# Optimization experiments

Hardware: AMD Instinct MI355X
Metric: run time of the kernel (lower is better)

Reference implementation:

```python
import jax, jax.numpy as jnp
import numpy as np
from jax import lax

B, L, H = 32, 512, 1024
PRED_LEN = 32
LN_EPS = 1e-5


def setup_inputs() -> dict:
    key = jax.random.key(0)
    k1, k2, k3 = jax.random.split(key, 3)
    x = jax.random.normal(k1, (B, L, H), dtype=jnp.float32)
    # scale recurrent/input weights by 1/sqrt(H) so the linear recurrence stays finite
    Wxh = jax.random.normal(k2, (H, H), dtype=jnp.float32) / jnp.sqrt(jnp.float32(H))
    Whh = jax.random.normal(k3, (H, H), dtype=jnp.float32) / jnp.sqrt(jnp.float32(H))
    ln_w = jnp.ones((H,), dtype=jnp.float32)
    ln_b = jnp.zeros((H,), dtype=jnp.float32)
    return {"x": x, "Wxh": Wxh, "Whh": Whh, "ln_w": ln_w, "ln_b": ln_b, "pred_len": PRED_LEN}


def _layer_norm(y, w, b):
    mu = jnp.mean(y, axis=-1, keepdims=True)
    var = jnp.mean(jnp.square(y - mu), axis=-1, keepdims=True)
    return (y - mu) * lax.rsqrt(var + LN_EPS) * w + b


def reference(x, Wxh, Whh, ln_w, ln_b, pred_len):
    b, l, h = x.shape
    # precompute input projections for all timesteps: x_t @ Wxh^T (nn.Linear convention)
    xW = jnp.einsum('blh,kh->lbk', x, Wxh)  # [L, B, H]
    WhhT = Whh.T

    def rec_step(h_t, xw_t):
        h_t = xw_t + h_t @ WhhT
        return h_t, h_t

    h0 = jnp.zeros((b, h), dtype=x.dtype)
    h_last, rec = lax.scan(rec_step, h0, xW)
    rec = jnp.transpose(rec, (1, 0, 2))  # [B, L, H]

    def pred_step(h_t, _):
        h_t = h_t @ WhhT
        return h_t, h_t

    _, outs = lax.scan(pred_step, h_last, None, length=pred_len)
    outs = jnp.transpose(outs, (1, 0, 2))  # [B, pred_len, H]
    outputs = _layer_norm(outs, ln_w, ln_b)
    return rec, outputs
```

## Files before the change

kernel.cpp:

```cpp
#include <hip/hip_runtime.h>

#define BB 32
#define LL 512
#define HH 1024
#define PRED 32
#define CC 16
#define NC (LL / CC)
#define C8 8
#define NC8 (LL / C8)
#define LN_EPS 1e-5f

typedef short bf16x8 __attribute__((ext_vector_type(8)));
typedef short s16x4  __attribute__((ext_vector_type(4)));
typedef float f32x4  __attribute__((ext_vector_type(4)));

static __device__ __forceinline__ void split3(float x, short& h, short& m, short& l) {
    unsigned u = __float_as_uint(x);
    unsigned rh = (u + 0x7fffu + ((u >> 16) & 1u)) & 0xffff0000u;
    h = (short)(rh >> 16);
    float x1 = x - __uint_as_float(rh);
    unsigned u1 = __float_as_uint(x1);
    unsigned rm = (u1 + 0x7fffu + ((u1 >> 16) & 1u)) & 0xffff0000u;
    m = (short)(rm >> 16);
    float x2 = x1 - __uint_as_float(rm);
    unsigned u2 = __float_as_uint(x2);
    unsigned rl = (u2 + 0x7fffu + ((u2 >> 16) & 1u)) & 0xffff0000u;
    l = (short)(rl >> 16);
}

static __device__ __forceinline__ void split2(float x, short& h, short& m) {
    unsigned u = __float_as_uint(x);
    unsigned rh = (u + 0x7fffu + ((u >> 16) & 1u)) & 0xffff0000u;
    h = (short)(rh >> 16);
    float x1 = x - __uint_as_float(rh);
    unsigned u1 = __float_as_uint(x1);
    unsigned rm = (u1 + 0x7fffu + ((u1 >> 16) & 1u)) & 0xffff0000u;
    m = (short)(rm >> 16);
}

#define MFMA6(ACC, AH, AM, AL, BH, BM, BL) \
    ACC = __builtin_amdgcn_mfma_f32_16x16x32_bf16(AL, BH, ACC, 0, 0, 0); \
    ACC = __builtin_amdgcn_mfma_f32_16x16x32_bf16(AH, BL, ACC, 0, 0, 0); \
    ACC = __builtin_amdgcn_mfma_f32_16x16x32_bf16(AM, BM, ACC, 0, 0, 0); \
    ACC = __builtin_amdgcn_mfma_f32_16x16x32_bf16(AM, BH, ACC, 0, 0, 0); \
    ACC = __builtin_amdgcn_mfma_f32_16x16x32_bf16(AH, BM, ACC, 0, 0, 0); \
    ACC = __builtin_amdgcn_mfma_f32_16x16x32_bf16(AH, BH, ACC, 0, 0, 0);

__global__ __launch_bounds__(256) void transpose_k(const float* __restrict__ in,
                                                   float* __restrict__ out) {
    __shared__ float tile[32][33];
    int bx = blockIdx.x * 32, by = blockIdx.y * 32;
    int tx = threadIdx.x, ty = threadIdx.y;
    #pragma unroll
    for (int i = 0; i < 32; i += 8)
        tile[ty + i][tx] = in[(size_t)(by + ty + i) * HH + bx + tx];
    __syncthreads();
    #pragma unroll
    for (int i = 0; i < 32; i += 8)
        out[(size_t)(bx + ty + i) * HH + by + tx] = tile[tx][ty + i];
}
// ... 103 lines not shown
            vh0[j] = h; vm0[j] = m;
            split2(xs[j + 8], h, m);
            vh1[j] = h; vm1[j] = m;
        }
        *(bf16x8*)&As2[0][ar][akc]     = vh0;
        *(bf16x8*)&As2[0][ar][akc + 8] = vh1;
        *(bf16x8*)&As2[1][ar][akc]     = vm0;
        *(bf16x8*)&As2[1][ar][akc + 8] = vm1;
        *(bf16x8*)&Bs2[bp][bnr][bkh]     = rb0;
        *(bf16x8*)&Bs2[bp][bnr][bkh + 8] = rb1;
        __syncthreads();
        if (kt + 32 < HH) {
            const float* An = Arow + kt + 32;
            av0 = *(const float4*)(An);
            av1 = *(const float4*)(An + 4);
            av2 = *(const float4*)(An + 8);
            av3 = *(const float4*)(An + 12);
            const short* Bn = Brow + kt + 32;
            rb0 = *(const bf16x8*)(Bn);
            rb1 = *(const bf16x8*)(Bn + 8);
        }
        bf16x8 ah[2], am[2];
        #pragma unroll
        for (int i = 0; i < 2; ++i) {
            ah[i] = *(const bf16x8*)&As2[0][w * 32 + i * 16 + fr][fk];
            am[i] = *(const bf16x8*)&As2[1][w * 32 + i * 16 + fr][fk];
        }
        #pragma unroll
        for (int j = 0; j < 4; ++j) {
            bf16x8 bh = *(const bf16x8*)&Bs2[0][j * 16 + fr][fk];
            bf16x8 bm = *(const bf16x8*)&Bs2[1][j * 16 + fr][fk];
            #pragma unroll
            for (int i = 0; i < 2; ++i) {
                f32x4 a = acc[i][j];
                a = __builtin_amdgcn_mfma_f32_16x16x32_bf16(am[i], bm, a, 0, 0, 0);
                a = __builtin_amdgcn_mfma_f32_16x16x32_bf16(am[i], bh, a, 0, 0, 0);
                a = __builtin_amdgcn_mfma_f32_16x16x32_bf16(ah[i], bm, a, 0, 0, 0);
                a = __builtin_amdgcn_mfma_f32_16x16x32_bf16(ah[i], bh, a, 0, 0, 0);
                acc[i][j] = a;
            }
        }
        __syncthreads();
    }
    const int orow = (lane >> 4) * 4;
    #pragma unroll
    for (int i = 0; i < 2; ++i)
        #pragma unroll
        for (int j = 0; j < 4; ++j) {
            int c = n0 + j * 16 + fr;
            #pragma unroll
            for (int reg = 0; reg < 4; ++reg) {
                int r = m0 + w * 32 + i * 16 + orow + reg;
                C[(size_t)r * HH + c] = acc[i][j][reg];
            }
        }
}

__global__ __launch_bounds__(128) void step_p(
    const short* __restrict__ SA, long sab, long sac, long psA,
    const short* __restrict__ SB,
    float* __restrict__ O, long sob, long soc, int add,
    float* __restrict__ P, long spb, long spc,
    short* __restrict__ S, long ssb, long ssc, long psS) {
    const size_t HM = (size_t)HH * HH;
    __shared__ __align__(16) short As[3][32][40];
    __shared__ __align__(16) short Bs[3][64][40];
    const int tid = threadIdx.x;
    const int lane = tid & 63;
    const int w = tid >> 6;
    const int n0 = blockIdx.x * 64;
    const int m0 = blockIdx.y * 32;
    const int ar = tid >> 2;
    const int akc = (tid & 3) * 8;
    const int agr = m0 + ar;
    const short* Arow = SA + (long)(agr & 31) * sab + (long)(agr >> 5) * sac + akc;
    const int bnr = tid & 63;
    const int bkh = (tid >> 6) * 16;
    const short* Brow = SB + (size_t)(n0 + bnr) * HH + bkh;
    const int fr = lane & 15;
    const int fk = (lane >> 4) * 8;

    f32x4 acc00 = 0, acc01 = 0, acc10 = 0, acc11 = 0;

    bf16x8 ra0 = *(const bf16x8*)(Arow);
    bf16x8 ra1 = *(const bf16x8*)(Arow + psA);
    bf16x8 ra2 = *(const bf16x8*)(Arow + 2 * psA);
    bf16x8 rb0 = *(const bf16x8*)(Brow);
    bf16x8 rb1 = *(const bf16x8*)(Brow + 8);
    bf16x8 rb2 = *(const bf16x8*)(Brow + HM);
    bf16x8 rb3 = *(const bf16x8*)(Brow + HM + 8);
    bf16x8 rb4 = *(const bf16x8*)(Brow + 2 * HM);
    bf16x8 rb5 = *(const bf16x8*)(Brow + 2 * HM + 8);

    for (int kt = 0; kt < HH; kt += 32) {
        *(bf16x8*)&As[0][ar][akc] = ra0;
        *(bf16x8*)&As[1][ar][akc] = ra1;
        *(bf16x8*)&As[2][ar][akc] = ra2;
        *(bf16x8*)&Bs[0][bnr][bkh] = rb0;
        *(bf16x8*)&Bs[0][bnr][bkh + 8] = rb1;
        *(bf16x8*)&Bs[1][bnr][bkh] = rb2;
        *(bf16x8*)&Bs[1][bnr][bkh + 8] = rb3;
        *(bf16x8*)&Bs[2][bnr][bkh] = rb4;
        *(bf16x8*)&Bs[2][bnr][bkh + 8] = rb5;
        __syncthreads();
        if (kt + 32 < HH) {
            const short* An = Arow + kt + 32;
            const short* Bn = Brow + kt + 32;
            ra0 = *(const bf16x8*)(An);
            ra1 = *(const bf16x8*)(An + psA);
            ra2 = *(const bf16x8*)(An + 2 * psA);
            rb0 = *(const bf16x8*)(Bn);
            rb1 = *(const bf16x8*)(Bn + 8);
            rb2 = *(const bf16x8*)(Bn + HM);
            rb3 = *(const bf16x8*)(Bn + HM + 8);
            rb4 = *(const bf16x8*)(Bn + 2 * HM);
            rb5 = *(const bf16x8*)(Bn + 2 * HM + 8);
        }
        bf16x8 a00 = *(const bf16x8*)&As[0][fr][fk];
        bf16x8 a01 = *(const bf16x8*)&As[0][16 + fr][fk];
        bf16x8 a10 = *(const bf16x8*)&As[1][fr][fk];
        bf16x8 a11 = *(const bf16x8*)&As[1][16 + fr][fk];
        bf16x8 a20 = *(const bf16x8*)&As[2][fr][fk];
        bf16x8 a21 = *(const bf16x8*)&As[2][16 + fr][fk];
        bf16x8 b00 = *(const bf16x8*)&Bs[0][w * 32 + fr][fk];
        bf16x8 b01 = *(const bf16x8*)&Bs[0][w * 32 + 16 + fr][fk];
        bf16x8 b10 = *(const bf16x8*)&Bs[1][w * 32 + fr][fk];
        bf16x8 b11 = *(const bf16x8*)&Bs[1][w * 32 + 16 + fr][fk];
        bf16x8 b20 = *(const bf16x8*)&Bs[2][w * 32 + fr][fk];
        bf16x8 b21 = *(const bf16x8*)&Bs[2][w * 32 + 16 + fr][fk];
        MFMA6(acc00, a00, a10, a20, b00, b10, b20)
        MFMA6(acc01, a00, a10, a20, b01, b11, b21)
        MFMA6(acc10, a01, a11, a21, b00, b10, b20)
        MFMA6(acc11, a01, a11, a21, b01, b11, b21)
        __syncthreads();
    }
    const int orow = (lane >> 4) * 4;
    #pragma unroll
    for (int mf = 0; mf < 2; ++mf) {
        #pragma unroll
        for (int nf = 0; nf < 2; ++nf) {
            f32x4 v = mf == 0 ? (nf == 0 ? acc00 : acc01) : (nf == 0 ? acc10 : acc11);
            int c = n0 + w * 32 + nf * 16 + fr;
            #pragma unroll
            for (int reg = 0; reg < 4; ++reg) {
                int r = m0 + mf * 16 + orow + reg;
                long rb = (long)(r & 31), rc = (long)(r >> 5);
                float val = v[reg];
                if (O) {
                    float* p = O + rb * sob + rc * soc + c;
                    if (add) val += *p;
                    *p = val;
                }
                if (P) {
                    float* q = P + rb * spb + rc * spc + c;
                    *q += val;
                }
                if (S) {
                    short h, m, l;
                    split3(val, h, m, l);
                    short* s = S + rb * ssb + rc * ssc + c;
                    s[0] = h; s[psS] = m; s[2 * psS] = l;
                }
            }
        }
    }
}

__global__ __launch_bounds__(256) void step_p64(
    const short* __restrict__ SA, long sab, long sac, long psA,
    const short* __restrict__ SB,
    float* __restrict__ O, long sob, long soc, int add,
    float* __restrict__ P, long spb, long spc,
    short* __restrict__ S, long ssb, long ssc, long psS,
    int nrows) {
    const size_t HM = (size_t)HH * HH;
    __shared__ __align__(16) short As[3][64][40];
    __shared__ __align__(16) short Bs[3][64][40];
    const int tid = threadIdx.x;
    const int lane = tid & 63;
    const int w = tid >> 6;
    const int wr = w & 1;
    const int wc = w >> 1;
    const int n0 = blockIdx.x * 64;
    const int m0 = blockIdx.y * 64;
    const int ar = tid >> 2;
    const int akc = (tid & 3) * 8;
    const int agr = m0 + ar;
    const short* Arow = SA + (long)(agr & 31) * sab + (long)(agr >> 5) * sac + akc;
    const short* Brow = SB + (size_t)(n0 + ar) * HH + akc;
    const int fr = lane & 15;
    const int fk = (lane >> 4) * 8;

    f32x4 acc00 = 0, acc01 = 0, acc10 = 0, acc11 = 0;

    bf16x8 ra0 = *(const bf16x8*)(Arow);
    bf16x8 ra1 = *(const bf16x8*)(Arow + psA);
    bf16x8 ra2 = *(const bf16x8*)(Arow + 2 * psA);
    bf16x8 rb0 = *(const bf16x8*)(Brow);
    bf16x8 rb1 = *(const bf16x8*)(Brow + HM);
    bf16x8 rb2 = *(const bf16x8*)(Brow + 2 * HM);

    for (int kt = 0; kt < HH; kt += 32) {
        *(bf16x8*)&As[0][ar][akc] = ra0;
        *(bf16x8*)&As[1][ar][akc] = ra1;
        *(bf16x8*)&As[2][ar][akc] = ra2;
        *(bf16x8*)&Bs[0][ar][akc] = rb0;
        *(bf16x8*)&Bs[1][ar][akc] = rb1;
        *(bf16x8*)&Bs[2][ar][akc] = rb2;
        __syncthreads();
        if (kt + 32 < HH) {
            const short* An = Arow + kt + 32;
            const short* Bn = Brow + kt + 32;
            ra0 = *(const bf16x8*)(An);
            ra1 = *(const bf16x8*)(An + psA);
            ra2 = *(const bf16x8*)(An + 2 * psA);
            rb0 = *(const bf16x8*)(Bn);
            rb1 = *(const bf16x8*)(Bn + HM);
            rb2 = *(const bf16x8*)(Bn + 2 * HM);
        }
        bf16x8 a00 = *(const bf16x8*)&As[0][wr * 32 + fr][fk];
        bf16x8 a01 = *(const bf16x8*)&As[0][wr * 32 + 16 + fr][fk];
        bf16x8 a10 = *(const bf16x8*)&As[1][wr * 32 + fr][fk];
        bf16x8 a11 = *(const bf16x8*)&As[1][wr * 32 + 16 + fr][fk];
        bf16x8 a20 = *(const bf16x8*)&As[2][wr * 32 + fr][fk];
        bf16x8 a21 = *(const bf16x8*)&As[2][wr * 32 + 16 + fr][fk];
        bf16x8 b00 = *(const bf16x8*)&Bs[0][wc * 32 + fr][fk];
        bf16x8 b01 = *(const bf16x8*)&Bs[0][wc * 32 + 16 + fr][fk];
        bf16x8 b10 = *(const bf16x8*)&Bs[1][wc * 32 + fr][fk];
        bf16x8 b11 = *(const bf16x8*)&Bs[1][wc * 32 + 16 + fr][fk];
        bf16x8 b20 = *(const bf16x8*)&Bs[2][wc * 32 + fr][fk];
        bf16x8 b21 = *(const bf16x8*)&Bs[2][wc * 32 + 16 + fr][fk];
        MFMA6(acc00, a00, a10, a20, b00, b10, b20)
        MFMA6(acc01, a00, a10, a20, b01, b11, b21)
        MFMA6(acc10, a01, a11, a21, b00, b10, b20)
        MFMA6(acc11, a01, a11, a21, b01, b11, b21)
        __syncthreads();
    }
    const int orow = (lane >> 4) * 4;
    #pragma unroll
    for (int mf = 0; mf < 2; ++mf) {
        #pragma unroll
        for (int nf = 0; nf < 2; ++nf) {
            f32x4 v = mf == 0 ? (nf == 0 ? acc00 : acc01) : (nf == 0 ? acc10 : acc11);
            int c = n0 + wc * 32 + nf * 16 + fr;
            #pragma unroll
            for (int reg = 0; reg < 4; ++reg) {
                int r = m0 + wr * 32 + mf * 16 + orow + reg;
                if (r >= nrows) continue;
                long rb = (long)(r & 31), rc = (long)(r >> 5);
                float val = v[reg];
                if (O) {
                    float* p = O + rb * sob + rc * soc + c;
                    if (add) val += *p;
                    *p = val;
                }
                if (P) {
                    float* q = P + rb * spb + rc * spc + c;
                    *q += val;
                }
                if (S) {
                    short h, m, l;
                    split3(val, h, m, l);
                    short* s = S + rb * ssb + rc * ssc + c;
                    s[0] = h; s[psS] = m; s[2 * psS] = l;
                }
            }
        }
    }
}

__global__ __launch_bounds__(512) void step_p128(
    const short* __restrict__ SA, long sab, long sac, long psA,
    const short* __restrict__ SB,
    float* __restrict__ O, long sob, long soc, int add,
    float* __restrict__ P, long spb, long spc,
    short* __restrict__ S, long ssb, long ssc, long psS,
    int nrows) {
    const size_t HM = (size_t)HH * HH;
    __shared__ __align__(16) short As[3][128][40];
    __shared__ __align__(16) short Bs[3][64][40];
    const int tid = threadIdx.x;
    const int lane = tid & 63;
    const int w = tid >> 6;
    const int wr = w & 3;
    const int wc = w >> 2;
    const int n0 = blockIdx.x * 64;
    const int m0 = blockIdx.y * 128;
    const int ar = tid >> 2;
    const int akc = (tid & 3) * 8;
    const int agr = m0 + ar;
    const short* Arow = SA + (long)(agr & 31) * sab + (long)(agr >> 5) * sac + akc;
    const bool bst = (tid < 384);
    const int bp = (tid >> 7) == 3 ? 2 : (tid >> 7);
    const int bt = tid & 127;
    const int bnr = bt >> 1;
    const int bkh = (bt & 1) * 16;
    const short* Brow = SB + (size_t)bp * HM + (size_t)(n0 + bnr) * HH + bkh;
    const int fr = lane & 15;
    const int fk = (lane >> 4) * 8;

    f32x4 acc00 = 0, acc01 = 0, acc10 = 0, acc11 = 0;

    bf16x8 ra0 = *(const bf16x8*)(Arow);
    bf16x8 ra1 = *(const bf16x8*)(Arow + psA);
    bf16x8 ra2 = *(const bf16x8*)(Arow + 2 * psA);
    bf16x8 rb0 = {}, rb1 = {};
    if (bst) { rb0 = *(const bf16x8*)(Brow); rb1 = *(const bf16x8*)(Brow + 8); }

    for (int kt = 0; kt < HH; kt += 32) {
        *(bf16x8*)&As[0][ar][akc] = ra0;
        *(bf16x8*)&As[1][ar][akc] = ra1;
        *(bf16x8*)&As[2][ar][akc] = ra2;
        if (bst) {
            *(bf16x8*)&Bs[bp][bnr][bkh]     = rb0;
            *(bf16x8*)&Bs[bp][bnr][bkh + 8] = rb1;
        }
        __syncthreads();
        if (kt + 32 < HH) {
            const short* An = Arow + kt + 32;
            ra0 = *(const bf16x8*)(An);
            ra1 = *(const bf16x8*)(An + psA);
            ra2 = *(const bf16x8*)(An + 2 * psA);
            if (bst) {
                const short* Bn = Brow + kt + 32;
                rb0 = *(const bf16x8*)(Bn);
                rb1 = *(const bf16x8*)(Bn + 8);
            }
        }
        bf16x8 a00 = *(const bf16x8*)&As[0][wr * 32 + fr][fk];
        bf16x8 a01 = *(const bf16x8*)&As[0][wr * 32 + 16 + fr][fk];
        bf16x8 a10 = *(const bf16x8*)&As[1][wr * 32 + fr][fk];
        bf16x8 a11 = *(const bf16x8*)&As[1][wr * 32 + 16 + fr][fk];
        bf16x8 a20 = *(const bf16x8*)&As[2][wr * 32 + fr][fk];
        bf16x8 a21 = *(const bf16x8*)&As[2][wr * 32 + 16 + fr][fk];
        bf16x8 b00 = *(const bf16x8*)&Bs[0][wc * 32 + fr][fk];
        bf16x8 b01 = *(const bf16x8*)&Bs[0][wc * 32 + 16 + fr][fk];
        bf16x8 b10 = *(const bf16x8*)&Bs[1][wc * 32 + fr][fk];
        bf16x8 b11 = *(const bf16x8*)&Bs[1][wc * 32 + 16 + fr][fk];
        bf16x8 b20 = *(const bf16x8*)&Bs[2][wc * 32 + fr][fk];
        bf16x8 b21 = *(const bf16x8*)&Bs[2][wc * 32 + 16 + fr][fk];
        MFMA6(acc00, a00, a10, a20, b00, b10, b20)
        MFMA6(acc01, a00, a10, a20, b01, b11, b21)
        MFMA6(acc10, a01, a11, a21, b00, b10, b20)
        MFMA6(acc11, a01, a11, a21, b01, b11, b21)
        __syncthreads();
    }
    const int orow = (lane >> 4) * 4;
    #pragma unroll
    for (int mf = 0; mf < 2; ++mf) {
        #pragma unroll
        for (int nf = 0; nf < 2; ++nf) {
            f32x4 v = mf == 0 ? (nf == 0 ? acc00 : acc01) : (nf == 0 ? acc10 : acc11);
            int c = n0 + wc * 32 + nf * 16 + fr;
            #pragma unroll
            for (int reg = 0; reg < 4; ++reg) {
                int r = m0 + wr * 32 + mf * 16 + orow + reg;
                if (r >= nrows) continue;
                long rb = (long)(r & 31), rc = (long)(r >> 5);
                float val = v[reg];
                if (O) {
                    float* p = O + rb * sob + rc * soc + c;
                    if (add) val += *p;
                    *p = val;
                }
                if (P) {
                    float* q = P + rb * spb + rc * spc + c;
                    *q += val;
                }
                if (S) {
                    short h, m, l;
                    split3(val, h, m, l);
                    short* s = S + rb * ssb + rc * ssc + c;
                    s[0] = h; s[psS] = m; s[2 * psS] = l;
                }
            }
        }
    }
}

__global__ __launch_bounds__(256) void ln_k(float* __restrict__ y,
                                            const float* __restrict__ w,
                                            const float* __restrict__ bia) {
    __shared__ float red[8];
    int row = blockIdx.x;
    float* p = y + (size_t)row * HH;
    int i4 = threadIdx.x * 4;
    float4 v = *(const float4*)&p[i4];
    float s = v.x + v.y + v.z + v.w;
    #pragma unroll
    for (int o = 32; o > 0; o >>= 1) s += __shfl_down(s, o, 64);
    int wid = threadIdx.x >> 6;
    if ((threadIdx.x & 63) == 0) red[wid] = s;
    __syncthreads();
    if (threadIdx.x == 0) red[4] = (red[0] + red[1] + red[2] + red[3]) * (1.f / HH);
    __syncthreads();
    float mu = red[4];
    float dx = v.x - mu, dy = v.y - mu, dz = v.z - mu, dw = v.w - mu;
    float q = dx * dx + dy * dy + dz * dz + dw * dw;
    #pragma unroll
    for (int o = 32; o > 0; o >>= 1) q += __shfl_down(q, o, 64);
    if ((threadIdx.x & 63) == 0) red[wid] = q;
    __syncthreads();
    if (threadIdx.x == 0) red[5] = (red[0] + red[1] + red[2] + red[3]) * (1.f / HH);
    __syncthreads();
    float rs = rsqrtf(red[5] + LN_EPS);
    float4 o4;
    o4.x = dx * rs * w[i4 + 0] + bia[i4 + 0];
    o4.y = dy * rs * w[i4 + 1] + bia[i4 + 1];
    o4.z = dz * rs * w[i4 + 2] + bia[i4 + 2];
    o4.w = dw * rs * w[i4 + 3] + bia[i4 + 3];
    *(float4*)&p[i4] = o4;
}

extern "C" void kernel_launch(void* const* d_in, const int* in_sizes, int n_in,
                              void* d_out, int out_size, void* d_ws, size_t ws_size,
                              hipStream_t stream) {
    const float* x    = (const float*)d_in[0];
    const float* Wxh  = (const float*)d_in[1];
    const float* Whh  = (const float*)d_in[2];
    const float* ln_w = (const float*)d_in[3];
    const float* ln_b = (const float*)d_in[4];

    const size_t MiB = 1024 * 1024;
    const long HM = (long)HH * HH;
    const long PS2 = 2048L * HH;
    float* rec  = (float*)d_out;
    float* outp = rec + (size_t)BB * LL * HH;

    const long LH  = (long)LL * HH;
    const long PB  = (long)PRED * HH;
    const long RS  = (long)HH;
    const long RC  = 32L * HH;
    float* nulf = (float*)nullptr;
    short* nuls = (short*)nullptr;
    char* wsb = (char*)d_ws;

    if (ws_size >= 64 * MiB) {
        const long CH8 = (long)C8 * HH;
        float* TP   = (float*)(wsb);
        short* SAP  = (short*)(wsb + 4 * MiB);
        short* SA0  = (short*)(wsb + 10 * MiB);
        short* SA1  = (short*)(wsb + 22 * MiB);
        short* SBM  = (short*)(wsb + 34 * MiB);
        short* SB8  = (short*)(wsb + 40 * MiB);
        short* SB16 = (short*)(wsb + 46 * MiB);
        short* SBr0 = (short*)(wsb + 52 * MiB);
        short* SBr1 = (short*)(wsb + 58 * MiB);

        transpose_k<<<dim3(32, 32), dim3(32, 8), 0, stream>>>(Whh, TP);
        split_a<<<dim3(1, HH), 256, 0, stream>>>(Wxh, RS, RC, SBr0, RS, RC, HM);
        gemm_mx<<<dim3(16, 128), 256, 0, stream>>>(x, SBr0, rec);
        split_a<<<dim3(1, HH), 256, 0, stream>>>(TP, RS, RC, SAP, RS, RC, HM);
        split_t<<<dim3(32, 32), dim3(32, 8), 0, stream>>>(TP, SBM);

        #define SQ64(SAi, SBi, Sot) \
            step_p64<<<dim3(16, 16), 256, 0, stream>>>(SAi, RS, RC, HM, SBi, \
                TP, RS, RC, 0, nulf, 0, 0, Sot, RS, RC, HM, 1024)
        SQ64(SAP, SBM, SA1);
        split_t<<<dim3(32, 32), dim3(32, 8), 0, stream>>>(TP, SBr0);
        SQ64(SA1, SBr0, SAP);
        split_t<<<dim3(32, 32), dim3(32, 8), 0, stream>>>(TP, SBr1);
        SQ64(SAP, SBr1, SA1);
        split_t<<<dim3(32, 32), dim3(32, 8), 0, stream>>>(TP, SB8);
        SQ64(SA1, SB8, SAP);
        split_t<<<dim3(32, 32), dim3(32, 8), 0, stream>>>(TP, SB16);

        split_a<<<dim3(1, 2048), 256, 0, stream>>>(rec, LH, CH8, SA0, RS, RC, PS2);
        for (int o = 1; o < C8; ++o) {
            short* Ain = (o & 1) ? SA0 : SA1;
            short* Sot = (o & 1) ? SA1 : SA0;
            step_p128<<<dim3(16, 16), 512, 0, stream>>>(Ain, RS, RC, PS2, SBM,
                rec + (size_t)o * HH, LH, CH8, 1, nulf, 0, 0,
                Sot, RS, RC, PS2, 2048);
        }

        #define SCAN(SRC, DST, T, SBpow) do { \
            int rows_ = (NC8 - (T)) * 32; \
            step_p128<<<dim3(16, (rows_ + 127) / 128), 512, 0, stream>>>( \
                SRC, RS, RC, PS2, SBpow, \
                rec + (size_t)((T) * C8 + C8 - 1) * HH, LH, CH8, 1, \
                nulf, 0, 0, DST + (size_t)(T) * RC, RS, RC, PS2, rows_); \
            copy_splits<<<(T) * 32, 256, 0, stream>>>(SRC, DST, PS2); \
        } while (0)
        #define SQI(SBi, SBo, last) do { \
            step_p64<<<dim3(16, 16), 256, 0, stream>>>(SAP, RS, RC, HM, SBi, \
                TP, RS, RC, 0, nulf, 0, 0, nuls, 0, 0, HM, 1024); \
            split_t<<<dim3(32, 32), dim3(32, 8), 0, stream>>>(TP, SBo); \
            if (!(last)) split_a<<<dim3(1, HH), 256, 0, stream>>>(TP, RS, RC, SAP, RS, RC, HM); \
        } while (0)

        SCAN(SA1, SA0, 1, SB8);
        SQI(SB16, SBr0, 0);
        SCAN(SA0, SA1, 2, SB16);
        SQI(SBr0, SBr1, 0);
        SCAN(SA1, SA0, 4, SBr0);
        SQI(SBr1, SBr0, 0);
        SCAN(SA0, SA1, 8, SBr1);
        SQI(SBr0, SBr1, 1);
        SCAN(SA1, SA0, 16, SBr0);
        SCAN(SA0, SA1, 32, SBr1);

        for (int o = 0; o < C8 - 1; ++o) {
            short* Ain = (o & 1) ? SA0 : SA1;
            short* Sot = (o & 1) ? SA1 : SA0;
            step_p128<<<dim3(16, 16), 512, 0, stream>>>(Ain, RS, RC, PS2, SBM,
                nulf, 0, 0, 0,
                rec + (size_t)(C8 + o) * HH, LH, CH8,
                (o == C8 - 2) ? nuls : Sot, RS, RC, PS2, 2016);
        }

        step_p<<<dim3(16, 1), 128, 0, stream>>>(SA1 + 63 * RC, RS, 0, PS2, SBM,
            outp, PB, 0, 0, nulf, 0, 0, SA0, RS, 0, PS2);
        step_p<<<dim3(16, 1), 128, 0, stream>>>(SA0, RS, 0, PS2, SBM,
            outp + HH, PB, 0, 0, nulf, 0, 0, SA0 + RC, RS, 0, PS2);
        tr_splits<<<dim3(32, 32, 3), dim3(32, 8), 0, stream>>>(SBM, SAP);
        SQ64(SAP, SBM, nuls);
        split_t<<<dim3(32, 32), dim3(32, 8), 0, stream>>>(TP, SBr0);
        step_p<<<dim3(16, 2), 128, 0, stream>>>(SA0, RS, RC, PS2, SBr0,
            outp + 2 * HH, PB, RS, 0, nulf, 0, 0,
            SA0 + 2 * RC, RS, RC, PS2);
        split_a<<<dim3(1, HH), 256, 0, stream>>>(TP, RS, RC, SAP, RS, RC, HM);
        SQ64(SAP, SBr0, nuls);
        split_t<<<dim3(32, 32), dim3(32, 8), 0, stream>>>(TP, SBr1);
        step_p<<<dim3(16, 4), 128, 0, stream>>>(SA0, RS, RC, PS2, SBr1,
            outp + 4 * HH, PB, RS, 0, nulf, 0, 0,
            SA0 + 4 * RC, RS, RC, PS2);
        step_p<<<dim3(16, 8), 128, 0, stream>>>(SA0, RS, RC, PS2, SB8,
            outp + 8 * HH, PB, RS, 0, nulf, 0, 0,
            SA0 + 8 * RC, RS, RC, PS2);
        step_p64<<<dim3(16, 8), 256, 0, stream>>>(SA0, RS, RC, PS2, SB16,
            outp + 16 * HH, PB, RS, 0, nulf, 0, 0,
            nuls, 0, 0, PS2, 512);
        #undef SQ64
        #undef SCAN
        #undef SQI

        ln_k<<<BB * PRED, 256, 0, stream>>>(outp, ln_w, ln_b);
        return;
    }

    const long CH = (long)CC * HH;
    float* TP   = (float*)(wsb);
    short* SAP  = (short*)(wsb + 4 * MiB);
    short* SA0  = (short*)(wsb + 10 * MiB);
    short* SA1  = (short*)(wsb + 16 * MiB);
    short* SBM  = (short*)(wsb + 22 * MiB);
    short* SBP  = (short*)(wsb + 28 * MiB);

    #define STEP64(SAx, sab, sac, SBx, Ox, sob, soc, addx, Px, spb, spc, Sx, ssb, ssc, NR) \
        step_p64<<<dim3(16, ((NR) + 63) / 64), 256, 0, stream>>>(SAx, sab, sac, HM, SBx, \
            Ox, sob, soc, addx, Px, spb, spc, Sx, ssb, ssc, HM, NR)
    #define STEP32(SAx, sab, sac, SBx, Ox, sob, soc, addx, Px, spb, spc, Sx, ssb, ssc, MG) \
        step_p<<<dim3(16, MG), 128, 0, stream>>>(SAx, sab, sac, HM, SBx, \
            Ox, sob, soc, addx, Px, spb, spc, Sx, ssb, ssc, HM)

    if (ws_size >= 52 * MiB) {
        short* SB2 = (short*)(wsb + 34 * MiB);
        short* SB4 = (short*)(wsb + 40 * MiB);
        short* SB8b = (short*)(wsb + 46 * MiB);

        transpose_k<<<dim3(32, 32), dim3(32, 8), 0, stream>>>(Whh, TP);
        split_a<<<dim3(1, HH), 256, 0, stream>>>(Wxh, RS, RC, SB2, RS, RC, HM);
        gemm_mx<<<dim3(16, 128), 256, 0, stream>>>(x, SB2, rec);
        split_a<<<dim3(1, HH), 256, 0, stream>>>(TP, RS, RC, SAP, RS, RC, HM);
        split_t<<<dim3(32, 32), dim3(32, 8), 0, stream>>>(TP, SBM);

        STEP64(SAP, RS, RC, SBM, TP, RS, RC, 0, nulf, 0, 0, SA0, RS, RC, 1024);
        split_t<<<dim3(32, 32), dim3(32, 8), 0, stream>>>(TP, SB2);
        STEP64(SA0, RS, RC, SB2, TP, RS, RC, 0, nulf, 0, 0, SAP, RS, RC, 1024);
        split_t<<<dim3(32, 32), dim3(32, 8), 0, stream>>>(TP, SB4);
        STEP64(SAP, RS, RC, SB4, TP, RS, RC, 0, nulf, 0, 0, SA0, RS, RC, 1024);
        split_t<<<dim3(32, 32), dim3(32, 8), 0, stream>>>(TP, SB8b);
        STEP64(SA0, RS, RC, SB8b, TP, RS, RC, 0, nulf, 0, 0, nuls, 0, 0, 1024);
        split_t<<<dim3(32, 32), dim3(32, 8), 0, stream>>>(TP, SBP);

        split_a<<<dim3(1, HH), 256, 0, stream>>>(rec, LH, CH, SA0, RS, RC, HM);
        for (int o = 1; o < CC; ++o) {
            short* Ain = (o & 1) ? SA0 : SA1;
            short* Sot = (o & 1) ? SA1 : SA0;
            STEP64(Ain, RS, RC, SBM,
                   rec + (size_t)o * HH, LH, CH, 1, nulf, 0, 0,
                   Sot, RS, RC, 1024);
        }
        for (int c = 1; c < NC; ++c)
            STEP32(SA1 + (size_t)(c - 1) * 32 * HH, RS, 0, SBP,
                   rec + ((size_t)c * CC + CC - 1) * HH, LH, 0, 1, nulf, 0, 0,
                   SA1 + (size_t)c * 32 * HH, RS, 0, 1);
        for (int o = 0; o < CC - 1; ++o) {
            short* Ain = (o & 1) ? SA0 : SA1;
            short* Sot = (o & 1) ? SA1 : SA0;
            STEP64(Ain, RS, RC, SBM,
                   nulf, 0, 0, 0,
                   rec + (size_t)(CC + o) * HH, LH, CH,
                   (o == CC - 2) ? nuls : Sot, RS, RC, 992);
        }
        STEP32(SA1 + (size_t)992 * HH, RS, 0, SBM, outp, PB, 0, 0, nulf, 0, 0, SA0, RS, 0, 1);
        STEP32(SA0, RS, 0, SBM, outp + HH, PB, 0, 0, nulf, 0, 0, SA0 + (size_t)32 * HH, RS, 0, 1);
        STEP32(SA0, RS, RC, SB2, outp + 2 * HH, PB, RS, 0, nulf, 0, 0, SA0 + (size_t)2 * 32 * HH, RS, RC, 2);
        STEP32(SA0, RS, RC, SB4, outp + 4 * HH, PB, RS, 0, nulf, 0, 0, SA0 + (size_t)4 * 32 * HH, RS, RC, 4);
        STEP32(SA0, RS, RC, SB8b, outp + 8 * HH, PB, RS, 0, nulf, 0, 0, SA0 + (size_t)8 * 32 * HH, RS, RC, 8);
        STEP64(SA0, RS, RC, SBP, outp + 16 * HH, PB, RS, 0, nulf, 0, 0, nuls, 0, 0, 512);

        ln_k<<<BB * PRED, 256, 0, stream>>>(outp, ln_w, ln_b);
        return;
    }

    transpose_k<<<dim3(32, 32), dim3(32, 8), 0, stream>>>(Whh, TP);
    split_a<<<dim3(1, HH), 256, 0, stream>>>(Wxh, RS, RC, SBP, RS, RC, HM);
    gemm_mx<<<dim3(16, 128), 256, 0, stream>>>(x, SBP, rec);
    split_a<<<dim3(1, HH), 256, 0, stream>>>(TP, RS, RC, SAP, RS, RC, HM);
    split_t<<<dim3(32, 32), dim3(32, 8), 0, stream>>>(TP, SBM);

    STEP64(SAP, RS, RC, SBM, TP, RS, RC, 0, nulf, 0, 0, SA0, RS, RC, 1024);
    split_t<<<dim3(32, 32), dim3(32, 8), 0, stream>>>(TP, SBP);
    STEP64(SA0, RS, RC, SBP, TP, RS, RC, 0, nulf, 0, 0, SAP, RS, RC, 1024);
    split_t<<<dim3(32, 32), dim3(32, 8), 0, stream>>>(TP, SBP);
    STEP64(SAP, RS, RC, SBP, TP, RS, RC, 0, nulf, 0, 0, SA0, RS, RC, 1024);
    split_t<<<dim3(32, 32), dim3(32, 8), 0, stream>>>(TP, SBP);
    STEP64(SA0, RS, RC, SBP, TP, RS, RC, 0, nulf, 0, 0, nuls, 0, 0, 1024);
    split_t<<<dim3(32, 32), dim3(32, 8), 0, stream>>>(TP, SBP);

    split_a<<<dim3(1, HH), 256, 0, stream>>>(rec, LH, CH, SA0, RS, RC, HM);
    for (int o = 1; o < CC; ++o) {
        short* Ain = (o & 1) ? SA0 : SA1;
        short* Sot = (o & 1) ? SA1 : SA0;
        STEP64(Ain, RS, RC, SBM,
               rec + (size_t)o * HH, LH, CH, 1, nulf, 0, 0,
               Sot, RS, RC, 1024);
    }
    for (int c = 1; c < NC; ++c)
        STEP32(SA1 + (size_t)(c - 1) * 32 * HH, RS, 0, SBP,
               rec + ((size_t)c * CC + CC - 1) * HH, LH, 0, 1, nulf, 0, 0,
               SA1 + (size_t)c * 32 * HH, RS, 0, 1);
    for (int o = 0; o < CC - 1; ++o) {
        short* Ain = (o & 1) ? SA0 : SA1;
        short* Sot = (o & 1) ? SA1 : SA0;
        STEP64(Ain, RS, RC, SBM,
               nulf, 0, 0, 0,
               rec + (size_t)(CC + o) * HH, LH, CH,
               (o == CC - 2) ? nuls : Sot, RS, RC, 992);
    }
    STEP32(SA1 + (size_t)992 * HH, RS, 0, SBM, outp, PB, 0, 0, nulf, 0, 0, SA0, RS, 0, 1);
    STEP32(SA0, RS, 0, SBM, outp + HH, PB, 0, 0, nulf, 0, 0, SA0 + (size_t)32 * HH, RS, 0, 1);
    tr_splits<<<dim3(32, 32, 3), dim3(32, 8), 0, stream>>>(SBM, SAP);
    STEP64(SAP, RS, RC, SBM, TP, RS, RC, 0, nulf, 0, 0, SA1, RS, RC, 1024);
    split_t<<<dim3(32, 32), dim3(32, 8), 0, stream>>>(TP, SBP);
    STEP32(SA0, RS, RC, SBP, outp + 2 * HH, PB, RS, 0, nulf, 0, 0, SA0 + (size_t)2 * 32 * HH, RS, RC, 2);
    STEP64(SA1, RS, RC, SBP, TP, RS, RC, 0, nulf, 0, 0, SAP, RS, RC, 1024);
    split_t<<<dim3(32, 32), dim3(32, 8), 0, stream>>>(TP, SBP);
    STEP32(SA0, RS, RC, SBP, outp + 4 * HH, PB, RS, 0, nulf, 0, 0, SA0 + (size_t)4 * 32 * HH, RS, RC, 4);
    STEP64(SAP, RS, RC, SBP, TP, RS, RC, 0, nulf, 0, 0, SA1, RS, RC, 1024);
    split_t<<<dim3(32, 32), dim3(32, 8), 0, stream>>>(TP, SBP);
    STEP32(SA0, RS, RC, SBP, outp + 8 * HH, PB, RS, 0, nulf, 0, 0, SA0 + (size_t)8 * 32 * HH, RS, RC, 8);
    STEP64(SA1, RS, RC, SBP, TP, RS, RC, 0, nulf, 0, 0, nuls, 0, 0, 1024);
    split_t<<<dim3(32, 32), dim3(32, 8), 0, stream>>>(TP, SBP);
    STEP64(SA0, RS, RC, SBP, outp + 16 * HH, PB, RS, 0, nulf, 0, 0, nuls, 0, 0, 512);

    ln_k<<<BB * PRED, 256, 0, stream>>>(outp, ln_w, ln_b);
    #undef STEP64
    #undef STEP32
}
```

Before: 1.502 ms.

## Batch multi-descriptor GEMM kernel and powers-of-Whh tail to cut sequential launches

Adds a step_b kernel that takes up to eight GEMM descriptors per launch, so several independent split-bf16 products (powers of Whh and the tail steps) run together in one grid. When workspace allows, it precomputes Whh^1..Whh^8 and higher powers, replaces the serial intra-chunk fix-up loop with one batched launch, and computes the prediction outputs using precomputed powers instead of a chain of steps. The aim is to shorten the serial critical path and reduce kernel-launch count. In exchange it needs about 124 MiB of workspace, does extra power-matrix GEMMs, and removes the old low-workspace fallback paths.

```diff
diff --git a/kernel.cpp b/kernel.cpp
--- a/kernel.cpp
+++ b/kernel.cpp
@@ -4,8 +4,6 @@
 #define LL 512
 #define HH 1024
 #define PRED 32
-#define CC 16
-#define NC (LL / CC)
 #define C8 8
 #define NC8 (LL / C8)
 #define LN_EPS 1e-5f
@@ -215,6 +213,112 @@
             for (int reg = 0; reg < 4; ++reg) {
                 int r = m0 + w * 32 + i * 16 + orow + reg;
                 C[(size_t)r * HH + c] = acc[i][j][reg];
+            }
+        }
+}
+
+struct GD  { const short* A; const short* B; float* O; float* P; short* S; };
+struct GD8 { GD g[8]; };
+
+__global__ __launch_bounds__(256) void step_b(
+    GD8 dsc, int ypg,
+    long sab, long sac, long psA,
+    long sob, long soc, int add,
+    long spb, long spc,
+    long ssb, long ssc, long psS,
+    int nrows) {
+    const size_t HM = (size_t)HH * HH;
+    __shared__ __align__(16) short As[3][128][40];
+    __shared__ __align__(16) short Bs[3][64][40];
+    const int tid = threadIdx.x;
+    const int lane = tid & 63;
+    const int w = tid >> 6;
+    const int grp = blockIdx.y / ypg;
+    const int yy  = blockIdx.y % ypg;
+    const int n0 = blockIdx.x * 64;
+    const int m0 = yy * 128;
+    const GD d = dsc.g[grp];
+    const int ar = tid >> 1;
+    const int akh = (tid & 1) * 16;
+    const int agr = m0 + ar;
+    const short* Arow = d.A + (long)(agr & 31) * sab + (long)(agr >> 5) * sac + akh;
+    const int br = tid >> 2;
+    const int bkc = (tid & 3) * 8;
+    const short* Brow = d.B + (size_t)(n0 + br) * HH + bkc;
+    const int fr = lane & 15;
+    const int fk = (lane >> 4) * 8;
+
+    f32x4 acc[2][4] = {};
+
+    bf16x8 ra[6], rb[3];
+    #pragma unroll
+    for (int p = 0; p < 3; ++p) {
+        ra[2 * p]     = *(const bf16x8*)(Arow + p * psA);
+        ra[2 * p + 1] = *(const bf16x8*)(Arow + p * psA + 8);
+        rb[p]         = *(const bf16x8*)(Brow + p * HM);
+    }
+    for (int kt = 0; kt < HH; kt += 32) {
+        #pragma unroll
+        for (int p = 0; p < 3; ++p) {
+            *(bf16x8*)&As[p][ar][akh]     = ra[2 * p];
+            *(bf16x8*)&As[p][ar][akh + 8] = ra[2 * p + 1];
+            *(bf16x8*)&Bs[p][br][bkc]     = rb[p];
+        }
+        __syncthreads();
+        if (kt + 32 < HH) {
+            #pragma unroll
+            for (int p = 0; p < 3; ++p) {
+                ra[2 * p]     = *(const bf16x8*)(Arow + p * psA + kt + 32);
+                ra[2 * p + 1] = *(const bf16x8*)(Arow + p * psA + kt + 40);
+                rb[p]         = *(const bf16x8*)(Brow + p * HM + kt + 32);
+            }
+        }
+        bf16x8 af[3][2], bfr[3][4];
+        #pragma unroll
+        for (int p = 0; p < 3; ++p) {
+            #pragma unroll
+            for (int mf = 0; mf < 2; ++mf)
+                af[p][mf] = *(const bf16x8*)&As[p][w * 32 + mf * 16 + fr][fk];
+            #pragma unroll
+            for (int nf = 0; nf < 4; ++nf)
+                bfr[p][nf] = *(const bf16x8*)&Bs[p][nf * 16 + fr][fk];
+        }
+        #pragma unroll
+        for (int mf = 0; mf < 2; ++mf)
+            #pragma unroll
+            for (int nf = 0; nf < 4; ++nf) {
+                MFMA6(acc[mf][nf], af[0][mf], af[1][mf], af[2][mf],
+                      bfr[0][nf], bfr[1][nf], bfr[2][nf])
+            }
+        __syncthreads();
+    }
+    const int orow = (lane >> 4) * 4;
+    #pragma unroll
+    for (int mf = 0; mf < 2; ++mf)
+        #pragma unroll
+        for (int nf = 0; nf < 4; ++nf) {
+            int c = n0 + nf * 16 + fr;
+            #pragma unroll
+            for (int reg = 0; reg < 4; ++reg) {
+                int r = m0 + w * 32 + mf * 16 + orow + reg;
+                if (r >= nrows) continue;
+                long rb_ = (long)(r & 31), rc_ = (long)(r >> 5);
+                float val = acc[mf][nf][reg];
+                if (d.O) {
+                    float* p = d.O + rb_ * sob + rc_ * soc + c;
+                    if (add) val += *p;
+                    *p = val;
+                }
+                if (d.P) {
+                    float* q = d.P + rb_ * spb + rc_ * spc + c;
+                    *q += val;
+                }
+                if (d.S) {
+                    short h, m, l;
+                    split3(val, h, m, l);
+                    short* s = d.S + rb_ * ssb + rc_ * ssc + c;
+                    s[0] = h; s[psS] = m; s[2 * psS] = l;
+                }
             }
         }
 }
@@ -242,9 +346,7 @@
     const short* Brow = SB + (size_t)(n0 + bnr) * HH + bkh;
     const int fr = lane & 15;
     const int fk = (lane >> 4) * 8;
-
     f32x4 acc00 = 0, acc01 = 0, acc10 = 0, acc11 = 0;
-
     bf16x8 ra0 = *(const bf16x8*)(Arow);
     bf16x8 ra1 = *(const bf16x8*)(Arow + psA);
     bf16x8 ra2 = *(const bf16x8*)(Arow + 2 * psA);
@@ -254,7 +356,6 @@
     bf16x8 rb3 = *(const bf16x8*)(Brow + HM + 8);
     bf16x8 rb4 = *(const bf16x8*)(Brow + 2 * HM);
     bf16x8 rb5 = *(const bf16x8*)(Brow + 2 * HM + 8);
-
     for (int kt = 0; kt < HH; kt += 32) {
         *(bf16x8*)&As[0][ar][akc] = ra0;
         *(bf16x8*)&As[1][ar][akc] = ra1;
@@ -314,10 +415,7 @@
                     if (add) val += *p;
                     *p = val;
                 }
-                if (P) {
-                    float* q = P + rb * spb + rc * spc + c;
-                    *q += val;
-                }
+                if (P) { float* q = P + rb * spb + rc * spc + c; *q += val; }
                 if (S) {
                     short h, m, l;
                     split3(val, h, m, l);
@@ -353,16 +451,13 @@
     const short* Brow = SB + (size_t)(n0 + ar) * HH + akc;
     const int fr = lane & 15;
     const int fk = (lane >> 4) * 8;
-
     f32x4 acc00 = 0, acc01 = 0, acc10 = 0, acc11 = 0;
-
     bf16x8 ra0 = *(const bf16x8*)(Arow);
     bf16x8 ra1 = *(const bf16x8*)(Arow + psA);
     bf16x8 ra2 = *(const bf16x8*)(Arow + 2 * psA);
     bf16x8 rb0 = *(const bf16x8*)(Brow);
     bf16x8 rb1 = *(const bf16x8*)(Brow + HM);
     bf16x8 rb2 = *(const bf16x8*)(Brow + 2 * HM);
-
     for (int kt = 0; kt < HH; kt += 32) {
         *(bf16x8*)&As[0][ar][akc] = ra0;
         *(bf16x8*)&As[1][ar][akc] = ra1;
@@ -417,10 +512,7 @@
                     if (add) val += *p;
                     *p = val;
                 }
-                if (P) {
-                    float* q = P + rb * spb + rc * spc + c;
-                    *q += val;
-                }
+                if (P) { float* q = P + rb * spb + rc * spc + c; *q += val; }
                 if (S) {
                     short h, m, l;
                     split3(val, h, m, l);
@@ -461,15 +553,12 @@
     const short* Brow = SB + (size_t)bp * HM + (size_t)(n0 + bnr) * HH + bkh;
     const int fr = lane & 15;
     const int fk = (lane >> 4) * 8;
-
     f32x4 acc00 = 0, acc01 = 0, acc10 = 0, acc11 = 0;
-
     bf16x8 ra0 = *(const bf16x8*)(Arow);
     bf16x8 ra1 = *(const bf16x8*)(Arow + psA);
     bf16x8 ra2 = *(const bf16x8*)(Arow + 2 * psA);
     bf16x8 rb0 = {}, rb1 = {};
     if (bst) { rb0 = *(const bf16x8*)(Brow); rb1 = *(const bf16x8*)(Brow + 8); }
-
     for (int kt = 0; kt < HH; kt += 32) {
         *(bf16x8*)&As[0][ar][akc] = ra0;
         *(bf16x8*)&As[1][ar][akc] = ra1;
@@ -526,10 +615,7 @@
                     if (add) val += *p;
                     *p = val;
                 }
-                if (P) {
-                    float* q = P + rb * spb + rc * spc + c;
-                    *q += val;
-                }
+                if (P) { float* q = P + rb * spb + rc * spc + c; *q += val; }
                 if (S) {
                     short h, m, l;
                     split3(val, h, m, l);
@@ -585,12 +671,13 @@
     const float* ln_b = (const float*)d_in[4];
 
     const size_t MiB = 1024 * 1024;
-    const long HM = (long)HH * HH;
+    const long HM  = (long)HH * HH;
     const long PS2 = 2048L * HH;
     float* rec  = (float*)d_out;
     float* outp = rec + (size_t)BB * LL * HH;
 
     const long LH  = (long)LL * HH;
+    const long CH8 = (long)C8 * HH;
     const long PB  = (long)PRED * HH;
     const long RS  = (long)HH;
     const long RC  = 32L * HH;
@@ -598,8 +685,108 @@
     short* nuls = (short*)nullptr;
     char* wsb = (char*)d_ws;
 
-    if (ws_size >= 64 * MiB) {
-        const long CH8 = (long)C8 * HH;
+    if (ws_size >= 124 * MiB) {
+        float* TP   = (float*)(wsb);
+        short* SBW  = (short*)(wsb + 4  * MiB);
+        float* T3a  = (float*)(wsb + 4  * MiB);
+        float* T3c  = (float*)(wsb + 8  * MiB);
+        float* T3e  = (float*)(wsb + 12 * MiB);
+        short* PW   = (short*)(wsb + 16 * MiB);
+        const size_t PWs = 3 * (size_t)HH * HH;
+        short* SB16 = (short*)(wsb + 64 * MiB);
+        short* SC32 = (short*)(wsb + 70 * MiB);
+        short* SC64 = (short*)(wsb + 76 * MiB);
+        short* SC128= (short*)(wsb + 82 * MiB);
+        short* SC256= (short*)(wsb + 88 * MiB);
+        short* SA0  = (short*)(wsb + 94 * MiB);
+        short* SA1  = (short*)(wsb + 106 * MiB);
+        short* SAP = (short*)(wsb + 94 * MiB);
+        short* SA2 = (short*)(wsb + 100 * MiB);
+        short* SA4 = (short*)(wsb + 106 * MiB);
+        short* SA6 = (short*)(wsb + 112 * MiB);
+
+        GD8 D{};
+        #define LAUNCH_B(NG, YPG, SAB, SAC, PSA, SOB, SOC, ADD, SPB, SPC, SSB, SSC, PSS, NR) \
+            step_b<<<dim3(16, (NG) * (YPG)), 256, 0, stream>>>(D, YPG, \
+                SAB, SAC, PSA, SOB, SOC, ADD, SPB, SPC, SSB, SSC, PSS, NR)
+        #define G1(AA, BS, OO, SS) do { D.g[0] = {AA, BS, OO, nulf, SS}; } while (0)
+
+        transpose_k<<<dim3(32, 32), dim3(32, 8), 0, stream>>>(Whh, TP);
+        split_a<<<dim3(1, HH), 256, 0, stream>>>(Wxh, RS, RC, SBW, RS, RC, HM);
+        gemm_mx<<<dim3(16, 128), 256, 0, stream>>>(x, SBW, rec);
+        split_a<<<dim3(1, HH), 256, 0, stream>>>(TP, RS, RC, SAP, RS, RC, HM);
+        split_t<<<dim3(32, 32), dim3(32, 8), 0, stream>>>(TP, PW);
+
+        G1(SAP, PW, TP, SA2);  LAUNCH_B(1, 8, RS, RC, HM, RS, RC, 0, 0, 0, RS, RC, HM, 1024);
+        split_t<<<dim3(32, 32), dim3(32, 8), 0, stream>>>(TP, PW + 1 * PWs);
+        G1(SA2, PW + 1 * PWs, TP, SA4);  LAUNCH_B(1, 8, RS, RC, HM, RS, RC, 0, 0, 0, RS, RC, HM, 1024);
+        split_t<<<dim3(32, 32), dim3(32, 8), 0, stream>>>(TP, PW + 3 * PWs);
+        D.g[0] = {SA2, PW, T3a, nulf, nuls};
+        D.g[1] = {SA4, PW, T3c, nulf, nuls};
+        D.g[2] = {SA4, PW + 1 * PWs, T3e, nulf, SA6};
+        LAUNCH_B(3, 8, RS, RC, HM, RS, RC, 0, 0, 0, RS, RC, HM, 1024);
+        split_t<<<dim3(32, 32), dim3(32, 8), 0, stream>>>(T3a, PW + 2 * PWs);
+        split_t<<<dim3(32, 32), dim3(32, 8), 0, stream>>>(T3c, PW + 4 * PWs);
+        split_t<<<dim3(32, 32), dim3(32, 8), 0, stream>>>(T3e, PW + 5 * PWs);
+        G1(SA6, PW, TP, nuls);  LAUNCH_B(1, 8, RS, RC, HM, RS, RC, 0, 0, 0, RS, RC, HM, 1024);
+        split_t<<<dim3(32, 32), dim3(32, 8), 0, stream>>>(TP, PW + 6 * PWs);
+        G1(SA4, PW + 3 * PWs, TP, SAP);  LAUNCH_B(1, 8, RS, RC, HM, RS, RC, 0, 0, 0, RS, RC, HM, 1024);
+        split_t<<<dim3(32, 32), dim3(32, 8), 0, stream>>>(TP, PW + 7 * PWs);
+        G1(SAP, PW + 7 * PWs, TP, SA2);  LAUNCH_B(1, 8, RS, RC, HM, RS, RC, 0, 0, 0, RS, RC, HM, 1024);
+        split_t<<<dim3(32, 32), dim3(32, 8), 0, stream>>>(TP, SB16);
+        G1(SA2, SB16, TP, SA4);  LAUNCH_B(1, 8, RS, RC, HM, RS, RC, 0, 0, 0, RS, RC, HM, 1024);
+        split_t<<<dim3(32, 32), dim3(32, 8), 0, stream>>>(TP, SC32);
+        G1(SA4, SC32, TP, SA2);  LAUNCH_B(1, 8, RS, RC, HM, RS, RC, 0, 0, 0, RS, RC, HM, 1024);
+        split_t<<<dim3(32, 32), dim3(32, 8), 0, stream>>>(TP, SC64);
+        G1(SA2, SC64, TP, SA4);  LAUNCH_B(1, 8, RS, RC, HM, RS, RC, 0, 0, 0, RS, RC, HM, 1024);
+        split_t<<<dim3(32, 32), dim3(32, 8), 0, stream>>>(TP, SC128);
+        G1(SA4, SC128, TP, nuls);  LAUNCH_B(1, 8, RS, RC, HM, RS, RC, 0, 0, 0, RS, RC, HM, 1024);
+        split_t<<<dim3(32, 32), dim3(32, 8), 0, stream>>>(TP, SC256);
+
+        split_a<<<dim3(1, 2048), 256, 0, stream>>>(rec, LH, CH8, SA0, RS, RC, PS2);
+        for (int o = 1; o < C8; ++o) {
+            short* Ain = (o & 1) ? SA0 : SA1;
+            short* Sot = (o & 1) ? SA1 : SA0;
+            step_p128<<<dim3(16, 16), 512, 0, stream>>>(Ain, RS, RC, PS2, PW,
+                rec + (size_t)o * HH, LH, CH8, 1, nulf, 0, 0,
+                Sot, RS, RC, PS2, 2048);
+        }
+
+        const short* SPOW[6] = {PW + 7 * PWs, SB16, SC32, SC64, SC128, SC256};
+        short* SRC = SA1; short* DST = SA0;
+        for (int s = 0; s < 6; ++s) {
+            int T = 1 << s;
+            int rows_ = (NC8 - T) * 32;
+            step_p128<<<dim3(16, (rows_ + 127) / 128), 512, 0, stream>>>(
+                SRC, RS, RC, PS2, SPOW[s],
+                rec + (size_t)(T * C8 + C8 - 1) * HH, LH, CH8, 1,
+                nulf, 0, 0, DST + (size_t)T * RC, RS, RC, PS2, rows_);
+            copy_splits<<<T * 32, 256, 0, stream>>>(SRC, DST, PS2);
+            short* t = SRC; SRC = DST; DST = t;
+        }
+        short* SFIN = SRC;
+        short* SFREE = DST;
+
+        for (int g = 0; g < 7; ++g)
+            D.g[g] = {SFIN, PW + (size_t)g * PWs, nulf, rec + (size_t)(C8 + g) * HH, nuls};
+        LAUNCH_B(7, 16, RS, RC, PS2, 0, 0, 0, LH, CH8, 0, 0, PS2, 2016);
+
+        for (int g = 0; g < 8; ++g)
+            D.g[g] = {SFIN + 63 * RC, PW + (size_t)g * PWs, outp + (size_t)g * HH,
+                      nulf, SFREE + (size_t)g * RC};
+        LAUNCH_B(8, 1, RS, 0, PS2, PB, 0, 0, 0, 0, RS, 0, PS2, 32);
+        G1(SFREE, PW + 7 * PWs, outp + 8 * HH, SFREE + 8 * RC);
+        LAUNCH_B(1, 2, RS, RC, PS2, PB, (long)HH, 0, 0, 0, RS, RC, PS2, 256);
+        G1(SFREE, SB16, outp + 16 * HH, nuls);
+        LAUNCH_B(1, 4, RS, RC, PS2, PB, (long)HH, 0, 0, 0, 0, 0, PS2, 512);
+        #undef LAUNCH_B
+        #undef G1
+
+        ln_k<<<BB * PRED, 256, 0, stream>>>(outp, ln_w, ln_b);
+        return;
+    }
+
+    {
         float* TP   = (float*)(wsb);
         short* SAP  = (short*)(wsb + 4 * MiB);
         short* SA0  = (short*)(wsb + 10 * MiB);
@@ -636,7 +823,6 @@
                 rec + (size_t)o * HH, LH, CH8, 1, nulf, 0, 0,
                 Sot, RS, RC, PS2, 2048);
         }
-
         #define SCAN(SRC, DST, T, SBpow) do { \
             int rows_ = (NC8 - (T)) * 32; \
             step_p128<<<dim3(16, (rows_ + 127) / 128), 512, 0, stream>>>( \
@@ -651,7 +837,6 @@
             split_t<<<dim3(32, 32), dim3(32, 8), 0, stream>>>(TP, SBo); \
             if (!(last)) split_a<<<dim3(1, HH), 256, 0, stream>>>(TP, RS, RC, SAP, RS, RC, HM); \
         } while (0)
-
         SCAN(SA1, SA0, 1, SB8);
         SQI(SB16, SBr0, 0);
         SCAN(SA0, SA1, 2, SB16);
@@ -662,7 +847,6 @@
         SQI(SBr0, SBr1, 1);
         SCAN(SA1, SA0, 16, SBr0);
         SCAN(SA0, SA1, 32, SBr1);
-
         for (int o = 0; o < C8 - 1; ++o) {
             short* Ain = (o & 1) ? SA0 : SA1;
             short* Sot = (o & 1) ? SA1 : SA0;
@@ -671,7 +855,6 @@
                 rec + (size_t)(C8 + o) * HH, LH, CH8,
                 (o == C8 - 2) ? nuls : Sot, RS, RC, PS2, 2016);
         }
-
         step_p<<<dim3(16, 1), 128, 0, stream>>>(SA1 + 63 * RC, RS, 0, PS2, SBM,
             outp, PB, 0, 0, nulf, 0, 0, SA0, RS, 0, PS2);
         step_p<<<dim3(16, 1), 128, 0, stream>>>(SA0, RS, 0, PS2, SBM,
@@ -699,127 +882,5 @@
         #undef SQI
 
         ln_k<<<BB * PRED, 256, 0, stream>>>(outp, ln_w, ln_b);
-        return;
-    }
-
-    const long CH = (long)CC * HH;
-    float* TP   = (float*)(wsb);
-    short* SAP  = (short*)(wsb + 4 * MiB);
-    short* SA0  = (short*)(wsb + 10 * MiB);
-    short* SA1  = (short*)(wsb + 16 * MiB);
-    short* SBM  = (short*)(wsb + 22 * MiB);
-    short* SBP  = (short*)(wsb + 28 * MiB);
-
-    #define STEP64(SAx, sab, sac, SBx, Ox, sob, soc, addx, Px, spb, spc, Sx, ssb, ssc, NR) \
-        step_p64<<<dim3(16, ((NR) + 63) / 64), 256, 0, stream>>>(SAx, sab, sac, HM, SBx, \
-            Ox, sob, soc, addx, Px, spb, spc, Sx, ssb, ssc, HM, NR)
-    #define STEP32(SAx, sab, sac, SBx, Ox, sob, soc, addx, Px, spb, spc, Sx, ssb, ssc, MG) \
-        step_p<<<dim3(16, MG), 128, 0, stream>>>(SAx, sab, sac, HM, SBx, \
-            Ox, sob, soc, addx, Px, spb, spc, Sx, ssb, ssc, HM)
-
-    if (ws_size >= 52 * MiB) {
-        short* SB2 = (short*)(wsb + 34 * MiB);
-        short* SB4 = (short*)(wsb + 40 * MiB);
-        short* SB8b = (short*)(wsb + 46 * MiB);
-
-        transpose_k<<<dim3(32, 32), dim3(32, 8), 0, stream>>>(Whh, TP);
-        split_a<<<dim3(1, HH), 256, 0, stream>>>(Wxh, RS, RC, SB2, RS, RC, HM);
-        gemm_mx<<<dim3(16, 128), 256, 0, stream>>>(x, SB2, rec);
-        split_a<<<dim3(1, HH), 256, 0, stream>>>(TP, RS, RC, SAP, RS, RC, HM);
-        split_t<<<dim3(32, 32), dim3(32, 8), 0, stream>>>(TP, SBM);
-
-        STEP64(SAP, RS, RC, SBM, TP, RS, RC, 0, nulf, 0, 0, SA0, RS, RC, 1024);
-        split_t<<<dim3(32, 32), dim3(32, 8), 0, stream>>>(TP, SB2);
-        STEP64(SA0, RS, RC, SB2, TP, RS, RC, 0, nulf, 0, 0, SAP, RS, RC, 1024);
-        split_t<<<dim3(32, 32), dim3(32, 8), 0, stream>>>(TP, SB4);
-        STEP64(SAP, RS, RC, SB4, TP, RS, RC, 0, nulf, 0, 0, SA0, RS, RC, 1024);
-        split_t<<<dim3(32, 32), dim3(32, 8), 0, stream>>>(TP, SB8b);
-        STEP64(SA0, RS, RC, SB8b, TP, RS, RC, 0, nulf, 0, 0, nuls, 0, 0, 1024);
-        split_t<<<dim3(32, 32), dim3(32, 8), 0, stream>>>(TP, SBP);
-
-        split_a<<<dim3(1, HH), 256, 0, stream>>>(rec, LH, CH, SA0, RS, RC, HM);
-        for (int o = 1; o < CC; ++o) {
-            short* Ain = (o & 1) ? SA0 : SA1;
-            short* Sot = (o & 1) ? SA1 : SA0;
-            STEP64(Ain, RS, RC, SBM,
-                   rec + (size_t)o * HH, LH, CH, 1, nulf, 0, 0,
-                   Sot, RS, RC, 1024);
-        }
-        for (int c = 1; c < NC; ++c)
-            STEP32(SA1 + (size_t)(c - 1) * 32 * HH, RS, 0, SBP,
-                   rec + ((size_t)c * CC + CC - 1) * HH, LH, 0, 1, nulf, 0, 0,
-                   SA1 + (size_t)c * 32 * HH, RS, 0, 1);
-        for (int o = 0; o < CC - 1; ++o) {
-            short* Ain = (o & 1) ? SA0 : SA1;
-            short* Sot = (o & 1) ? SA1 : SA0;
-            STEP64(Ain, RS, RC, SBM,
-                   nulf, 0, 0, 0,
-                   rec + (size_t)(CC + o) * HH, LH, CH,
-                   (o == CC - 2) ? nuls : Sot, RS, RC, 992);
-        }
-        STEP32(SA1 + (size_t)992 * HH, RS, 0, SBM, outp, PB, 0, 0, nulf, 0, 0, SA0, RS, 0, 1);
-        STEP32(SA0, RS, 0, SBM, outp + HH, PB, 0, 0, nulf, 0, 0, SA0 + (size_t)32 * HH, RS, 0, 1);
-        STEP32(SA0, RS, RC, SB2, outp + 2 * HH, PB, RS, 0, nulf, 0, 0, SA0 + (size_t)2 * 32 * HH, RS, RC, 2);
-        STEP32(SA0, RS, RC, SB4, outp + 4 * HH, PB, RS, 0, nulf, 0, 0, SA0 + (size_t)4 * 32 * HH, RS, RC, 4);
-        STEP32(SA0, RS, RC, SB8b, outp + 8 * HH, PB, RS, 0, nulf, 0, 0, SA0 + (size_t)8 * 32 * HH, RS, RC, 8);
-        STEP64(SA0, RS, RC, SBP, outp + 16 * HH, PB, RS, 0, nulf, 0, 0, nuls, 0, 0, 512);
-
-        ln_k<<<BB * PRED, 256, 0, stream>>>(outp, ln_w, ln_b);
-        return;
-    }
-
-    transpose_k<<<dim3(32, 32), dim3(32, 8), 0, stream>>>(Whh, TP);
-    split_a<<<dim3(1, HH), 256, 0, stream>>>(Wxh, RS, RC, SBP, RS, RC, HM);
-    gemm_mx<<<dim3(16, 128), 256, 0, stream>>>(x, SBP, rec);
-    split_a<<<dim3(1, HH), 256, 0, stream>>>(TP, RS, RC, SAP, RS, RC, HM);
-    split_t<<<dim3(32, 32), dim3(32, 8), 0, stream>>>(TP, SBM);
-
-    STEP64(SAP, RS, RC, SBM, TP, RS, RC, 0, nulf, 0, 0, SA0, RS, RC, 1024);
-    split_t<<<dim3(32, 32), dim3(32, 8), 0, stream>>>(TP, SBP);
-    STEP64(SA0, RS, RC, SBP, TP, RS, RC, 0, nulf, 0, 0, SAP, RS, RC, 1024);
-    split_t<<<dim3(32, 32), dim3(32, 8), 0, stream>>>(TP, SBP);
-    STEP64(SAP, RS, RC, SBP, TP, RS, RC, 0, nulf, 0, 0, SA0, RS, RC, 1024);
-    split_t<<<dim3(32, 32), dim3(32, 8), 0, stream>>>(TP, SBP);
-    STEP64(SA0, RS, RC, SBP, TP, RS, RC, 0, nulf, 0, 0, nuls, 0, 0, 1024);
-    split_t<<<dim3(32, 32), dim3(32, 8), 0, stream>>>(TP, SBP);
-
-    split_a<<<dim3(1, HH), 256, 0, stream>>>(rec, LH, CH, SA0, RS, RC, HM);
-    for (int o = 1; o < CC; ++o) {
-        short* Ain = (o & 1) ? SA0 : SA1;
-        short* Sot = (o & 1) ? SA1 : SA0;
-        STEP64(Ain, RS, RC, SBM,
-               rec + (size_t)o * HH, LH, CH, 1, nulf, 0, 0,
-               Sot, RS, RC, 1024);
-    }
-    for (int c = 1; c < NC; ++c)
-        STEP32(SA1 + (size_t)(c - 1) * 32 * HH, RS, 0, SBP,
-               rec + ((size_t)c * CC + CC - 1) * HH, LH, 0, 1, nulf, 0, 0,
-               SA1 + (size_t)c * 32 * HH, RS, 0, 1);
-    for (int o = 0; o < CC - 1; ++o) {
-        short* Ain = (o & 1) ? SA0 : SA1;
-        short* Sot = (o & 1) ? SA1 : SA0;
-        STEP64(Ain, RS, RC, SBM,
-               nulf, 0, 0, 0,
-               rec + (size_t)(CC + o) * HH, LH, CH,
-               (o == CC - 2) ? nuls : Sot, RS, RC, 992);
-    }
-    STEP32(SA1 + (size_t)992 * HH, RS, 0, SBM, outp, PB, 0, 0, nulf, 0, 0, SA0, RS, 0, 1);
-    STEP32(SA0, RS, 0, SBM, outp + HH, PB, 0, 0, nulf, 0, 0, SA0 + (size_t)32 * HH, RS, 0, 1);
-    tr_splits<<<dim3(32, 32, 3), dim3(32, 8), 0, stream>>>(SBM, SAP);
-    STEP64(SAP, RS, RC, SBM, TP, RS, RC, 0, nulf, 0, 0, SA1, RS, RC, 1024);
-    split_t<<<dim3(32, 32), dim3(32, 8), 0, stream>>>(TP, SBP);
-    STEP32(SA0, RS, RC, SBP, outp + 2 * HH, PB, RS, 0, nulf, 0, 0, SA0 + (size_t)2 * 32 * HH, RS, RC, 2);
-    STEP64(SA1, RS, RC, SBP, TP, RS, RC, 0, nulf, 0, 0, SAP, RS, RC, 1024);
-    split_t<<<dim3(32, 32), dim3(32, 8), 0, stream>>>(TP, SBP);
-    STEP32(SA0, RS, RC, SBP, outp + 4 * HH, PB, RS, 0, nulf, 0, 0, SA0 + (size_t)4 * 32 * HH, RS, RC, 4);
-    STEP64(SAP, RS, RC, SBP, TP, RS, RC, 0, nulf, 0, 0, SA1, RS, RC, 1024);
-    split_t<<<dim3(32, 32), dim3(32, 8), 0, stream>>>(TP, SBP);
-    STEP32(SA0, RS, RC, SBP, outp + 8 * HH, PB, RS, 0, nulf, 0, 0, SA0 + (size_t)8 * 32 * HH, RS, RC, 8);
-    STEP64(SA1, RS, RC, SBP, TP, RS, RC, 0, nulf, 0, 0, nuls, 0, 0, 1024);
-    split_t<<<dim3(32, 32), dim3(32, 8), 0, stream>>>(TP, SBP);
-    STEP64(SA0, RS, RC, SBP, outp + 16 * HH, PB, RS, 0, nulf, 0, 0, nuls, 0, 0, 512);
-
-    ln_k<<<BB * PRED, 256, 0, stream>>>(outp, ln_w, ln_b);
-    #undef STEP64
-    #undef STEP32
-}
+    }
+}
```

Result: no change. 1.498 ms (-0.2%).
